# Kernel optimization log

Hardware: AMD Instinct MI355X
Metric: run time of the kernel (lower is better)

Reference implementation:

```python
import jax, jax.numpy as jnp
import numpy as np

BATCH, SEQ, D_MODEL = 2, 2048, 1024
NUM_HEADS = 16
D_K = D_MODEL // NUM_HEADS  # 64
ROPE_THETA = 10000.0


def setup_inputs() -> dict:
    key = jax.random.key(0)
    ks = jax.random.split(key, 5)
    sigma = np.sqrt(2.0 / (D_MODEL + D_MODEL))
    return {
        "x": jax.random.normal(ks[0], (BATCH, SEQ, D_MODEL), dtype=jnp.float32),
        "Wq": jax.random.normal(ks[1], (D_MODEL, D_MODEL), dtype=jnp.float32) * sigma,
        "Wk": jax.random.normal(ks[2], (D_MODEL, D_MODEL), dtype=jnp.float32) * sigma,
        "Wv": jax.random.normal(ks[3], (D_MODEL, D_MODEL), dtype=jnp.float32) * sigma,
        "Wo": jax.random.normal(ks[4], (D_MODEL, D_MODEL), dtype=jnp.float32) * sigma,
        "token_positions": jnp.arange(SEQ, dtype=jnp.int32),
    }


def _rope(t, cos, sin):
    # t: [b, h, s, d_k]; cos/sin: [s, d_k//2]
    even, odd = t[..., ::2], t[..., 1::2]
    out_even = even * cos - odd * sin
    out_odd = odd * cos + even * sin
    return jnp.stack([out_even, out_odd], axis=-1).reshape(t.shape)


def reference(x, Wq, Wk, Wv, Wo, token_positions):
    b, s, d = x.shape
    h, dk = NUM_HEADS, D_K

    def split_heads(w):
        # Linear: einsum('... d_in, d_out d_in -> ... d_out')
        y = jnp.einsum('bsd,ed->bse', x, w)
        return y.reshape(b, s, h, dk).transpose(0, 2, 1, 3)  # [b,h,s,dk]

    q, k, v = split_heads(Wq), split_heads(Wk), split_heads(Wv)

    # RoPE tables from token positions
    inv_freq = 1.0 / (ROPE_THETA ** (jnp.arange(0, dk, 2, dtype=jnp.float32) / dk))
    freqs = token_positions.astype(jnp.float32)[:, None] * inv_freq[None, :]  # [s, dk/2]
    cos, sin = jnp.cos(freqs), jnp.sin(freqs)
    q = _rope(q, cos, sin)
    k = _rope(k, cos, sin)

    scale = 1.0 / jnp.sqrt(jnp.asarray(dk, dtype=x.dtype))
    scores = jnp.einsum('bhqd,bhkd->bhqk', q, k) * scale  # [b,h,s,s]
    causal = jnp.tril(jnp.ones((s, s), dtype=bool))
    scores = jnp.where(causal, scores, -jnp.inf)
    probs = jax.nn.softmax(scores, axis=-1)
    out = jnp.einsum('bhqk,bhkd->bhqd', probs, v)
    out = out.transpose(0, 2, 1, 3).reshape(b, s, d)
    return jnp.einsum('bsd,ed->bse', out, Wo)
```

## Files before the change

kernel.cpp:

```cpp
#include <hip/hip_runtime.h>
#include <hip/hip_bf16.h>


#define BATCH   2
#define SEQLEN  2048
#define DMODEL  1024
#define NHEADS  16
#define DK      64

typedef __attribute__((ext_vector_type(8))) short bf16x8;
typedef __attribute__((ext_vector_type(4))) short bf16x4;
typedef __attribute__((ext_vector_type(4))) float f32x4;

__device__ __forceinline__ void gload_lds16(const void* g, void* l) {
  __builtin_amdgcn_global_load_lds(
      (const __attribute__((address_space(1))) unsigned int*)g,
      (__attribute__((address_space(3))) unsigned int*)l, 16, 0, 0);
}

__device__ __forceinline__ float fast_exp2(float x) {
#if __has_builtin(__builtin_amdgcn_exp2f)
  return __builtin_amdgcn_exp2f(x);
#else
  return exp2f(x);
#endif
}

__global__ __launch_bounds__(256) void cast_all(
    const float* __restrict__ x,  const float* __restrict__ wq,
    const float* __restrict__ wk, const float* __restrict__ wv,
    const float* __restrict__ wo,
    __hip_bfloat16* __restrict__ xb,  __hip_bfloat16* __restrict__ wqb,
    __hip_bfloat16* __restrict__ wkb, __hip_bfloat16* __restrict__ wvb,
    __hip_bfloat16* __restrict__ wob) {
  const size_t MM = (size_t)1 << 20;
  size_t i = ((size_t)blockIdx.x * 256 + threadIdx.x) * 8;
  const float* src; __hip_bfloat16* dst; size_t off = i;
  if (i < 4 * MM)      { src = x;  dst = xb; }
  else if (i < 5 * MM) { src = wq; dst = wqb; off = i - 4 * MM; }
  else if (i < 6 * MM) { src = wk; dst = wkb; off = i - 5 * MM; }
  else if (i < 7 * MM) { src = wv; dst = wvb; off = i - 6 * MM; }
  else                 { src = wo; dst = wob; off = i - 7 * MM; }
  float4 a = *(const float4*)(src + off);
  float4 b = *(const float4*)(src + off + 4);
  __hip_bfloat16 t[8];
  t[0] = __float2bfloat16(a.x); t[1] = __float2bfloat16(a.y);
  t[2] = __float2bfloat16(a.z); t[3] = __float2bfloat16(a.w);
  t[4] = __float2bfloat16(b.x); t[5] = __float2bfloat16(b.y);
  t[6] = __float2bfloat16(b.z); t[7] = __float2bfloat16(b.w);
  *(bf16x8*)(dst + off) = *(const bf16x8*)t;
}

__device__ __forceinline__ void gemm_core(
    const __hip_bfloat16* __restrict__ A, const __hip_bfloat16* __restrict__ W,
    int bm, int bn, int K, f32x4 (&acc)[4][4]) {
  __shared__ __hip_bfloat16 As[128 * 32];
  __shared__ __hip_bfloat16 Ws[128 * 32];
  const int tid  = threadIdx.x;
  const int wave = tid >> 6, lane = tid & 63;
  const int col  = lane & 15, quad = lane >> 4;
  const int wm   = (wave & 1) * 64, wn = (wave >> 1) * 64;
  const int srow = wave * 32;
  const int l4   = lane >> 2, sl = lane & 3;

  for (int k0 = 0; k0 < K; k0 += 32) {
#pragma unroll
    for (int c = 0; c < 2; ++c) {
      int r = srow + c * 16 + l4;
      int g = sl ^ (r & 3);
      gload_lds16(A + (size_t)(bm + r) * K + k0 + g * 8, &As[(srow + c * 16) * 32]);
      gload_lds16(W + (size_t)(bn + r) * K + k0 + g * 8, &Ws[(srow + c * 16) * 32]);
    }
    __syncthreads();
    bf16x8 af[4], bfr[4];
#pragma unroll
    for (int mt = 0; mt < 4; ++mt) {
      int r = wm + mt * 16 + col;
      af[mt] = *(const bf16x8*)&As[r * 32 + ((quad ^ (r & 3)) * 8)];
    }
#pragma unroll
    for (int nt = 0; nt < 4; ++nt) {
      int r = wn + nt * 16 + col;
      bfr[nt] = *(const bf16x8*)&Ws[r * 32 + ((quad ^ (r & 3)) * 8)];
    }
#pragma unroll
    for (int mt = 0; mt < 4; ++mt)
#pragma unroll
      for (int nt = 0; nt < 4; ++nt)
        acc[mt][nt] = __builtin_amdgcn_mfma_f32_16x16x32_bf16(af[mt], bfr[nt], acc[mt][nt], 0, 0, 0);
    __syncthreads();
  }
}

__global__ __launch_bounds__(256) void mfma_qkv(
    const __hip_bfloat16* __restrict__ xb,
    const __hip_bfloat16* __restrict__ wqb,
    const __hip_bfloat16* __restrict__ wkb,
    const __hip_bfloat16* __restrict__ wvb,
    __hip_bfloat16* __restrict__ Qw,
    __hip_bfloat16* __restrict__ Kw,
    __hip_bfloat16* __restrict__ Vtw) {
  const int z = blockIdx.z;
  const __hip_bfloat16* W = (z == 0) ? wqb : (z == 1) ? wkb : wvb;
  const int bm = blockIdx.x * 128, bn = blockIdx.y * 128;
  f32x4 acc[4][4] = {};
  gemm_core(xb, W, bm, bn, DMODEL, acc);

  const int wave = threadIdx.x >> 6, lane = threadIdx.x & 63;
  const int col  = lane & 15, quad = lane >> 4;
  const int wm   = (wave & 1) * 64, wn = (wave >> 1) * 64;

  if (z < 2) {
    __hip_bfloat16* C = (z == 0) ? Qw : Kw;
#pragma unroll
    for (int mt = 0; mt < 4; ++mt)
#pragma unroll
      for (int nt = 0; nt < 4; ++nt) {
        int n = bn + wn + nt * 16 + col;
#pragma unroll
        for (int r = 0; r < 4; ++r) {
          int m = bm + wm + mt * 16 + quad * 4 + r;
          C[(size_t)m * DMODEL + n] = __float2bfloat16(acc[mt][nt][r]);
        }
      }
  } else {
#pragma unroll
    for (int mt = 0; mt < 4; ++mt)
#pragma unroll
      for (int nt = 0; nt < 4; ++nt) {
        int n  = bn + wn + nt * 16 + col;
        int m0 = bm + wm + mt * 16 + quad * 4;
        __hip_bfloat16 t[4];
#pragma unroll
        for (int r = 0; r < 4; ++r) t[r] = __float2bfloat16(acc[mt][nt][r]);
        size_t off = (((size_t)(m0 >> 11) * NHEADS + (n >> 6)) * DK + (n & 63)) * SEQLEN + (m0 & 2047);
        *(bf16x4*)(Vtw + off) = *(const bf16x4*)t;
      }
  }
}

__global__ __launch_bounds__(256) void mfma_out(
    const __hip_bfloat16* __restrict__ Ow,
    const __hip_bfloat16* __restrict__ wob,
    float* __restrict__ out) {
  const int bm = blockIdx.x * 128, bn = blockIdx.y * 128;
  f32x4 acc[4][4] = {};
  gemm_core(Ow, wob, bm, bn, DMODEL, acc);
  const int wave = threadIdx.x >> 6, lane = threadIdx.x & 63;
  const int col  = lane & 15, quad = lane >> 4;
  const int wm   = (wave & 1) * 64, wn = (wave >> 1) * 64;
#pragma unroll
  for (int mt = 0; mt < 4; ++mt)
#pragma unroll
    for (int nt = 0; nt < 4; ++nt) {
      int n = bn + wn + nt * 16 + col;
#pragma unroll
      for (int r = 0; r < 4; ++r) {
        int m = bm + wm + mt * 16 + quad * 4 + r;
        out[(size_t)m * DMODEL + n] = acc[mt][nt][r];
      }
    }
}

__global__ __launch_bounds__(256) void rope_kernel(
    __hip_bfloat16* __restrict__ Q,
    __hip_bfloat16* __restrict__ Kt,
    const int* __restrict__ pos, int npairs) {
  int idx = blockIdx.x * blockDim.x + threadIdx.x;
  if (idx >= npairs) return;
  int ip = idx & 511;
  int s  = (idx >> 9) & (SEQLEN - 1);
  int p  = ip & 31;
  float inv_freq = exp2f(-13.287712379549449f * ((float)(2 * p) / 64.0f));
  float ang = (float)pos[s] * inv_freq;
  float sn, cs;
  sincosf(ang, &sn, &cs);
  const float SCL = 0.18033688011112042f;
  size_t off = (size_t)idx * 2;
  float qe = __bfloat162float(Q[off]), qo = __bfloat162float(Q[off + 1]);
  Q[off]     = __float2bfloat16((qe * cs - qo * sn) * SCL);
  Q[off + 1] = __float2bfloat16((qo * cs + qe * sn) * SCL);
  float ke = __bfloat162float(Kt[off]), ko = __bfloat162float(Kt[off + 1]);
  Kt[off]     = __float2bfloat16(ke * cs - ko * sn);
  Kt[off + 1] = __float2bfloat16(ko * cs + ke * sn);
}

__global__ __launch_bounds__(512) void attn_mfma(
    const __hip_bfloat16* __restrict__ Q,
    const __hip_bfloat16* __restrict__ K,
    const __hip_bfloat16* __restrict__ Vt,
    __hip_bfloat16* __restrict__ O) {
  __shared__ __align__(16) __hip_bfloat16 Ks[2][64 * 64];
  __shared__ __align__(16) __hip_bfloat16 Vs[2][64 * 64];
  __shared__ __align__(16) __hip_bfloat16 Pl[8][32 * 64];
  const int lin  = (int)blockIdx.y * (int)gridDim.x + (int)blockIdx.x;
  const int xcd  = lin & 7, slot = lin >> 3;
  const int bh   = xcd * 4 + (slot & 3);
  const int strip = 15 - (slot >> 2);
  const int b = bh >> 4, h = bh & 15;
  const int wave = threadIdx.x >> 6;
  const int lane = threadIdx.x & 63;
  const int qg = wave & 3;
  const int kg = wave >> 2;
  const int col = lane & 15, quad = lane >> 4;
  const int q0w = strip * 128 + qg * 32;
  const int cswz = col & 7;

  const size_t qkbase = ((size_t)b * SEQLEN) * DMODEL + (size_t)h * DK;
  const size_t vbase  = (size_t)bh * DK * SEQLEN;
  __hip_bfloat16* pl = &Pl[wave][0];

  const int sr = ((int)threadIdx.x >> 3) & 63;
  const int sl = (int)threadIdx.x & 7;
  const int sgch = sl ^ (sr & 7);

  bf16x8 stK[2], stV[2];
  auto stage_load = [&](int p) {
    const int j0 = p * 128;
#pragma unroll
    for (int g = 0; g < 2; ++g) {
      stK[g] = *(const bf16x8*)(K + qkbase + (size_t)(j0 + g * 64 + sr) * DMODEL + sgch * 8);
      stV[g] = *(const bf16x8*)(Vt + vbase + (size_t)sr * SEQLEN + j0 + g * 64 + sgch * 8);
    }
  };
  auto stage_write = [&]() {
#pragma unroll
    for (int g = 0; g < 2; ++g) {
      *(bf16x8*)&Ks[g][sr * 64 + sl * 8] = stK[g];
      *(bf16x8*)&Vs[g][sr * 64 + sl * 8] = stV[g];
    }
  };

  bf16x8 qf[2][2];
#pragma unroll
  for (int qt = 0; qt < 2; ++qt)
#pragma unroll
    for (int kc = 0; kc < 2; ++kc)
      qf[qt][kc] = *(const bf16x8*)(Q + qkbase +
          (size_t)(q0w + qt * 16 + col) * DMODEL + kc * 32 + quad * 8);

  f32x4 acc[2][4] = {};
  float l_i[2] = {0.f, 0.f};

  const bool skip_last = (kg == 1) && (qg < 2);

  stage_load(0);
  stage_write();
  __syncthreads();

  for (int p = 0; p <= strip; ++p) {
    const bool pre  = p < strip;
    const bool last = p == strip;
    if (pre) stage_load(p + 1);

    if (!(last && skip_last)) {
      const int kb = p * 128 + kg * 64;

      f32x4 s[2][4] = {};
#pragma unroll
      for (int kt = 0; kt < 4; ++kt) {
        const int row = kt * 16 + col;
#pragma unroll
        for (int kc = 0; kc < 2; ++kc) {
          bf16x8 kf = *(const bf16x8*)&Ks[kg][row * 64 + (((kc * 4 + quad) ^ cswz) * 8)];
#pragma unroll
          for (int qt = 0; qt < 2; ++qt)
            s[qt][kt] = __builtin_amdgcn_mfma_f32_16x16x32_bf16(kf, qf[qt][kc], s[qt][kt], 0, 0, 0);
        }
      }

      if (last) {
#pragma unroll
        for (int qt = 0; qt < 2; ++qt) {
          const int q = q0w + qt * 16 + col;
#pragma unroll
          for (int kt = 0; kt < 4; ++kt)
#pragma unroll
            for (int r = 0; r < 4; ++r)
              if (kb + kt * 16 + quad * 4 + r > q) s[qt][kt][r] = -1e30f;
        }
      }

#pragma unroll
      for (int qt = 0; qt < 2; ++qt) {
#pragma unroll
        for (int kt = 0; kt < 4; ++kt) {
          __hip_bfloat16 tp[4];
#pragma unroll
          for (int r = 0; r < 4; ++r) {
            float pv = fast_exp2(s[qt][kt][r] - 24.0f);
            l_i[qt] += pv;
            tp[r] = __float2bfloat16(pv);
          }
          int c2 = ((kt << 1) | (quad >> 1)) ^ cswz;
          *(bf16x4*)(pl + (qt * 16 + col) * 64 + c2 * 8 + (quad & 1) * 4) = *(const bf16x4*)tp;
        }
      }

#pragma unroll
      for (int jc = 0; jc < 2; ++jc) {
        const int c2 = ((jc << 2) | quad) ^ cswz;
        bf16x8 pf[2];
#pragma unroll
        for (int qt = 0; qt < 2; ++qt)
          pf[qt] = *(const bf16x8*)(pl + (qt * 16 + col) * 64 + c2 * 8);
#pragma unroll
        for (int dt = 0; dt < 4; ++dt) {
          const int dv = dt * 16 + col;
          bf16x8 vf = *(const bf16x8*)&Vs[kg][dv * 64 + (((jc * 4 + quad) ^ cswz) * 8)];
#pragma unroll
          for (int qt = 0; qt < 2; ++qt)
            acc[qt][dt] = __builtin_amdgcn_mfma_f32_16x16x32_bf16(vf, pf[qt], acc[qt][dt], 0, 0, 0);
        }
      }
    }

    __syncthreads();
    if (pre) { stage_write(); __syncthreads(); }
  }

  float* accbuf = (float*)&Pl[0][0];
  float* lbuf   = (float*)&Ks[0][0];
  if (kg == 1) {
#pragma unroll
    for (int qt = 0; qt < 2; ++qt)
#pragma unroll
      for (int dt = 0; dt < 4; ++dt)
        *(f32x4*)(accbuf + ((qg * 8 + qt * 4 + dt) * 64 + lane) * 4) = acc[qt][dt];
    lbuf[(qg * 64 + lane) * 2 + 0] = l_i[0];
    lbuf[(qg * 64 + lane) * 2 + 1] = l_i[1];
  }
  __syncthreads();
  if (kg == 0) {
#pragma unroll
    for (int qt = 0; qt < 2; ++qt)
#pragma unroll
      for (int dt = 0; dt < 4; ++dt) {
        f32x4 o = *(const f32x4*)(accbuf + ((qg * 8 + qt * 4 + dt) * 64 + lane) * 4);
        acc[qt][dt] += o;
      }
    l_i[0] += lbuf[(qg * 64 + lane) * 2 + 0];
    l_i[1] += lbuf[(qg * 64 + lane) * 2 + 1];

#pragma unroll
    for (int qt = 0; qt < 2; ++qt) {
      float l = l_i[qt];
      l += __shfl_xor(l, 16, 64);
      l += __shfl_xor(l, 32, 64);
      const float inv = 1.f / l;
      const size_t orow = qkbase + (size_t)(q0w + qt * 16 + col) * DMODEL;
#pragma unroll
      for (int dt = 0; dt < 4; ++dt) {
        __hip_bfloat16 tp[4];
#pragma unroll
        for (int r = 0; r < 4; ++r) tp[r] = __float2bfloat16(acc[qt][dt][r] * inv);
        *(bf16x4*)(O + orow + dt * 16 + quad * 4) = *(const bf16x4*)tp;
      }
    }
  }
}

extern "C" void kernel_launch(void* const* d_in, const int* in_sizes, int n_in,
                              void* d_out, int out_size, void* d_ws, size_t ws_size,
                              hipStream_t stream) {
  const float* x  = (const float*)d_in[0];
  const float* Wq = (const float*)d_in[1];
  const float* Wk = (const float*)d_in[2];
  const float* Wv = (const float*)d_in[3];
  const float* Wo = (const float*)d_in[4];
  const int* pos  = (const int*)d_in[5];
  float* out = (float*)d_out;

  const size_t NELEM = (size_t)BATCH * SEQLEN * DMODEL;
  const size_t WELEM = (size_t)DMODEL * DMODEL;
  __hip_bfloat16* xb  = (__hip_bfloat16*)d_ws;
  __hip_bfloat16* Qw  = xb + NELEM;
  __hip_bfloat16* Kw  = Qw + NELEM;
  __hip_bfloat16* Vtw = Kw + NELEM;
  __hip_bfloat16* wqb = Vtw + NELEM;
  __hip_bfloat16* wkb = wqb + WELEM;
  __hip_bfloat16* wvb = wkb + WELEM;
  __hip_bfloat16* wob = wvb + WELEM;
  __hip_bfloat16* Ow  = xb;

  cast_all<<<4096, 256, 0, stream>>>(x, Wq, Wk, Wv, Wo, xb, wqb, wkb, wvb, wob);

  mfma_qkv<<<dim3(32, 8, 3), 256, 0, stream>>>(xb, wqb, wkb, wvb, Qw, Kw, Vtw);

  int npairs = BATCH * SEQLEN * (DMODEL / 2);
  rope_kernel<<<(npairs + 255) / 256, 256, 0, stream>>>(Qw, Kw, pos, npairs);

  attn_mfma<<<dim3(16, BATCH * NHEADS), 512, 0, stream>>>(Qw, Kw, Vtw, Ow);

  mfma_out<<<dim3(32, 8), 256, 0, stream>>>(Ow, wob, out);
}
```

Baseline: 185.3 us.

## Fuse fp32-to-bf16 casts into GEMM loads with register-staged double buffering

New measurement: 187.5 us. About the same (+1.2%).

```diff
diff --git a/kernel.cpp b/kernel.cpp
--- a/kernel.cpp
+++ b/kernel.cpp
@@ -11,12 +11,6 @@
 typedef __attribute__((ext_vector_type(8))) short bf16x8;
 typedef __attribute__((ext_vector_type(4))) short bf16x4;
 typedef __attribute__((ext_vector_type(4))) float f32x4;
-
-__device__ __forceinline__ void gload_lds16(const void* g, void* l) {
-  __builtin_amdgcn_global_load_lds(
-      (const __attribute__((address_space(1))) unsigned int*)g,
-      (__attribute__((address_space(3))) unsigned int*)l, 16, 0, 0);
-}
 
 __device__ __forceinline__ float fast_exp2(float x) {
 #if __has_builtin(__builtin_amdgcn_exp2f)
@@ -26,36 +20,26 @@
 #endif
 }
 
-__global__ __launch_bounds__(256) void cast_all(
-    const float* __restrict__ x,  const float* __restrict__ wq,
-    const float* __restrict__ wk, const float* __restrict__ wv,
-    const float* __restrict__ wo,
-    __hip_bfloat16* __restrict__ xb,  __hip_bfloat16* __restrict__ wqb,
-    __hip_bfloat16* __restrict__ wkb, __hip_bfloat16* __restrict__ wvb,
-    __hip_bfloat16* __restrict__ wob) {
-  const size_t MM = (size_t)1 << 20;
-  size_t i = ((size_t)blockIdx.x * 256 + threadIdx.x) * 8;
-  const float* src; __hip_bfloat16* dst; size_t off = i;
-  if (i < 4 * MM)      { src = x;  dst = xb; }
-  else if (i < 5 * MM) { src = wq; dst = wqb; off = i - 4 * MM; }
-  else if (i < 6 * MM) { src = wk; dst = wkb; off = i - 5 * MM; }
-  else if (i < 7 * MM) { src = wv; dst = wvb; off = i - 6 * MM; }
-  else                 { src = wo; dst = wob; off = i - 7 * MM; }
-  float4 a = *(const float4*)(src + off);
-  float4 b = *(const float4*)(src + off + 4);
+__device__ __forceinline__ bf16x8 load_cvt(const __hip_bfloat16* p) {
+  return *(const bf16x8*)p;
+}
+__device__ __forceinline__ bf16x8 load_cvt(const float* p) {
+  float4 a = *(const float4*)p;
+  float4 b = *(const float4*)(p + 4);
   __hip_bfloat16 t[8];
   t[0] = __float2bfloat16(a.x); t[1] = __float2bfloat16(a.y);
   t[2] = __float2bfloat16(a.z); t[3] = __float2bfloat16(a.w);
   t[4] = __float2bfloat16(b.x); t[5] = __float2bfloat16(b.y);
   t[6] = __float2bfloat16(b.z); t[7] = __float2bfloat16(b.w);
-  *(bf16x8*)(dst + off) = *(const bf16x8*)t;
-}
-
+  return *(const bf16x8*)t;
+}
+
+template <typename TA, typename TW>
 __device__ __forceinline__ void gemm_core(
-    const __hip_bfloat16* __restrict__ A, const __hip_bfloat16* __restrict__ W,
+    const TA* __restrict__ A, const TW* __restrict__ W,
     int bm, int bn, int K, f32x4 (&acc)[4][4]) {
-  __shared__ __hip_bfloat16 As[128 * 32];
-  __shared__ __hip_bfloat16 Ws[128 * 32];
+  __shared__ __hip_bfloat16 As[2][128 * 32];
+  __shared__ __hip_bfloat16 Ws[2][128 * 32];
   const int tid  = threadIdx.x;
   const int wave = tid >> 6, lane = tid & 63;
   const int col  = lane & 15, quad = lane >> 4;
@@ -63,48 +47,70 @@
   const int srow = wave * 32;
   const int l4   = lane >> 2, sl = lane & 3;
 
-  for (int k0 = 0; k0 < K; k0 += 32) {
+  bf16x8 ra[2], rw[2];
+  auto stage_load = [&](int k0) {
 #pragma unroll
     for (int c = 0; c < 2; ++c) {
       int r = srow + c * 16 + l4;
       int g = sl ^ (r & 3);
-      gload_lds16(A + (size_t)(bm + r) * K + k0 + g * 8, &As[(srow + c * 16) * 32]);
-      gload_lds16(W + (size_t)(bn + r) * K + k0 + g * 8, &Ws[(srow + c * 16) * 32]);
-    }
-    __syncthreads();
+      ra[c] = load_cvt(A + (size_t)(bm + r) * K + k0 + g * 8);
+      rw[c] = load_cvt(W + (size_t)(bn + r) * K + k0 + g * 8);
+    }
+  };
+  auto stage_write = [&](int buf) {
+#pragma unroll
+    for (int c = 0; c < 2; ++c) {
+      int r = srow + c * 16 + l4;
+      *(bf16x8*)&As[buf][r * 32 + sl * 8] = ra[c];
+      *(bf16x8*)&Ws[buf][r * 32 + sl * 8] = rw[c];
+    }
+  };
+
+  const int NK = K / 32;
+  stage_load(0);
+  stage_write(0);
+  __syncthreads();
+
+  for (int i = 0; i < NK; ++i) {
+    const int buf = i & 1;
+    const bool pre = (i + 1 < NK);
+    if (pre) stage_load((i + 1) * 32);
+
     bf16x8 af[4], bfr[4];
 #pragma unroll
     for (int mt = 0; mt < 4; ++mt) {
       int r = wm + mt * 16 + col;
-      af[mt] = *(const bf16x8*)&As[r * 32 + ((quad ^ (r & 3)) * 8)];
+      af[mt] = *(const bf16x8*)&As[buf][r * 32 + ((quad ^ (r & 3)) * 8)];
     }
 #pragma unroll
     for (int nt = 0; nt < 4; ++nt) {
       int r = wn + nt * 16 + col;
-      bfr[nt] = *(const bf16x8*)&Ws[r * 32 + ((quad ^ (r & 3)) * 8)];
+      bfr[nt] = *(const bf16x8*)&Ws[buf][r * 32 + ((quad ^ (r & 3)) * 8)];
     }
 #pragma unroll
     for (int mt = 0; mt < 4; ++mt)
 #pragma unroll
       for (int nt = 0; nt < 4; ++nt)
         acc[mt][nt] = __builtin_amdgcn_mfma_f32_16x16x32_bf16(af[mt], bfr[nt], acc[mt][nt], 0, 0, 0);
+
+    if (pre) stage_write(buf ^ 1);
     __syncthreads();
   }
 }
 
 __global__ __launch_bounds__(256) void mfma_qkv(
-    const __hip_bfloat16* __restrict__ xb,
-    const __hip_bfloat16* __restrict__ wqb,
-    const __hip_bfloat16* __restrict__ wkb,
-    const __hip_bfloat16* __restrict__ wvb,
+    const float* __restrict__ x,
+    const float* __restrict__ wq,
+    const float* __restrict__ wk,
+    const float* __restrict__ wv,
     __hip_bfloat16* __restrict__ Qw,
     __hip_bfloat16* __restrict__ Kw,
     __hip_bfloat16* __restrict__ Vtw) {
   const int z = blockIdx.z;
-  const __hip_bfloat16* W = (z == 0) ? wqb : (z == 1) ? wkb : wvb;
+  const float* W = (z == 0) ? wq : (z == 1) ? wk : wv;
   const int bm = blockIdx.x * 128, bn = blockIdx.y * 128;
   f32x4 acc[4][4] = {};
-  gemm_core(xb, W, bm, bn, DMODEL, acc);
+  gemm_core(x, W, bm, bn, DMODEL, acc);
 
   const int wave = threadIdx.x >> 6, lane = threadIdx.x & 63;
   const int col  = lane & 15, quad = lane >> 4;
@@ -141,11 +147,11 @@
 
 __global__ __launch_bounds__(256) void mfma_out(
     const __hip_bfloat16* __restrict__ Ow,
-    const __hip_bfloat16* __restrict__ wob,
+    const float* __restrict__ wo,
     float* __restrict__ out) {
   const int bm = blockIdx.x * 128, bn = blockIdx.y * 128;
   f32x4 acc[4][4] = {};
-  gemm_core(Ow, wob, bm, bn, DMODEL, acc);
+  gemm_core(Ow, wo, bm, bn, DMODEL, acc);
   const int wave = threadIdx.x >> 6, lane = threadIdx.x & 63;
   const int col  = lane & 15, quad = lane >> 4;
   const int wm   = (wave & 1) * 64, wn = (wave >> 1) * 64;
@@ -372,25 +378,17 @@
   float* out = (float*)d_out;
 
   const size_t NELEM = (size_t)BATCH * SEQLEN * DMODEL;
-  const size_t WELEM = (size_t)DMODEL * DMODEL;
-  __hip_bfloat16* xb  = (__hip_bfloat16*)d_ws;
-  __hip_bfloat16* Qw  = xb + NELEM;
+  __hip_bfloat16* Qw  = (__hip_bfloat16*)d_ws;
   __hip_bfloat16* Kw  = Qw + NELEM;
   __hip_bfloat16* Vtw = Kw + NELEM;
-  __hip_bfloat16* wqb = Vtw + NELEM;
-  __hip_bfloat16* wkb = wqb + WELEM;
-  __hip_bfloat16* wvb = wkb + WELEM;
-  __hip_bfloat16* wob = wvb + WELEM;
-  __hip_bfloat16* Ow  = xb;
-
-  cast_all<<<4096, 256, 0, stream>>>(x, Wq, Wk, Wv, Wo, xb, wqb, wkb, wvb, wob);
-
-  mfma_qkv<<<dim3(32, 8, 3), 256, 0, stream>>>(xb, wqb, wkb, wvb, Qw, Kw, Vtw);
+  __hip_bfloat16* Ow  = Vtw + NELEM;
+
+  mfma_qkv<<<dim3(32, 8, 3), 256, 0, stream>>>(x, Wq, Wk, Wv, Qw, Kw, Vtw);
 
   int npairs = BATCH * SEQLEN * (DMODEL / 2);
   rope_kernel<<<(npairs + 255) / 256, 256, 0, stream>>>(Qw, Kw, pos, npairs);
 
   attn_mfma<<<dim3(16, BATCH * NHEADS), 512, 0, stream>>>(Qw, Kw, Vtw, Ow);
 
-  mfma_out<<<dim3(32, 8), 256, 0, stream>>>(Ow, wob, out);
-}
+  mfma_out<<<dim3(32, 8), 256, 0, stream>>>(Ow, Wo, out);
+}
```
